# Optimization experiments

Measured on AMD Instinct MI355X. Metric: run time of the kernel, lower is better.

## Reference

```python
import jax, jax.numpy as jnp
import numpy as np

B, T, C, H = 4, 2048, 1024, 16
D = C // H  # head dim = 64


def setup_inputs() -> dict:
    key = jax.random.key(0)
    k0, k1, k2, k3, k4 = jax.random.split(key, 5)
    s = 0.02
    return {
        "x": jax.random.normal(k0, (B, T, C), dtype=jnp.float32),
        "W_qkv": jax.random.normal(k1, (C, 3 * C), dtype=jnp.float32) * s,
        "b_qkv": jnp.zeros((3 * C,), dtype=jnp.float32),
        "W_out": jax.random.normal(k2, (C, C), dtype=jnp.float32) * s,
        "b_out": jnp.zeros((C,), dtype=jnp.float32),
    }


def reference(x, W_qkv, b_qkv, W_out, b_out):
    b, t, c = x.shape
    qkv = x @ W_qkv + b_qkv                              # [B,T,3C]
    q, k, v = jnp.split(qkv, 3, axis=-1)
    # [B,T,C] -> [B,H,T,D]
    q = q.reshape(b, t, H, D).transpose(0, 2, 1, 3)
    k = k.reshape(b, t, H, D).transpose(0, 2, 1, 3)
    v = v.reshape(b, t, H, D).transpose(0, 2, 1, 3)
    scale = 1.0 / jnp.sqrt(jnp.asarray(D, dtype=q.dtype))
    attn = jnp.einsum("bhqd,bhkd->bhqk", q, k) * scale   # [B,H,T,T]
    causal = jnp.tril(jnp.ones((t, t), dtype=bool))
    attn = jnp.where(causal[None, None], attn, -jnp.inf)
    attn = jax.nn.softmax(attn, axis=-1)
    y = jnp.einsum("bhqk,bhkd->bhqd", attn, v)           # [B,H,T,D]
    y = y.transpose(0, 2, 1, 3).reshape(b, t, c)          # [B,T,C]
    return y @ W_out + b_out
```

## Files before the change

### kernel.cpp

```cpp
#include <hip/hip_runtime.h>
#include <math.h>

typedef __bf16 bf16x8 __attribute__((ext_vector_type(8)));
typedef __bf16 bf16x4 __attribute__((ext_vector_type(4)));
typedef short shortx4 __attribute__((ext_vector_type(4)));
typedef float floatx4 __attribute__((ext_vector_type(4)));

#define Tc 2048
#define Cdim 1024
#define Hc 16
#define Dc 64
#define Mrows 8192

__device__ __forceinline__ float bf2f(ushort u) {
  union { float f; unsigned int i; } v; v.i = ((unsigned int)u) << 16; return v.f;
}
__device__ __forceinline__ ushort f2bf(float f) {
  union { float f; unsigned int i; } v; v.f = f;
  unsigned int r = (v.i + 0x7FFFu + ((v.i >> 16) & 1u)) >> 16;
  return (ushort)r;
}
__device__ __forceinline__ ushort f2bf_pos(float f) {
  union { float f; unsigned int i; } v; v.f = f;
  return (ushort)((v.i + 0x8000u) >> 16);
}
__device__ __forceinline__ float exp2_fast(float x) {
#if __has_builtin(__builtin_amdgcn_exp2f)
  return __builtin_amdgcn_exp2f(x);
#else
  return exp2f(x);
#endif
}

#if __has_builtin(__builtin_amdgcn_mfma_f32_16x16x16_bf16)
__device__ __forceinline__ floatx4 mfma16(bf16x4 a, bf16x4 b, floatx4 c) {
  return __builtin_amdgcn_mfma_f32_16x16x16_bf16(a, b, c, 0, 0, 0);
}
#elif __has_builtin(__builtin_amdgcn_mfma_f32_16x16x16bf16_1k)
__device__ __forceinline__ floatx4 mfma16(bf16x4 a, bf16x4 b, floatx4 c) {
  union { bf16x4 bv; shortx4 sv; } ua, ub;
  ua.bv = a; ub.bv = b;
  return __builtin_amdgcn_mfma_f32_16x16x16bf16_1k(ua.sv, ub.sv, c, 0, 0, 0);
}
#else
__device__ __forceinline__ floatx4 mfma16(bf16x4 a, bf16x4 b, floatx4 c) {
  floatx4 d;
  asm("v_mfma_f32_16x16x16_bf16 %0, %1, %2, %3" : "=v"(d) : "v"(a), "v"(b), "v"(c));
  return d;
}
#endif

#if __has_builtin(__builtin_amdgcn_global_load_lds)
#define HAVE_GLL 1
__device__ __forceinline__ void async_load16(const ushort* g, ushort* l) {
  __builtin_amdgcn_global_load_lds((const __attribute__((address_space(1))) void*)g,
                                   (__attribute__((address_space(3))) void*)l, 16, 0, 0);
}
#else
#define HAVE_GLL 0
#endif

__global__ void sniff_kernel(const unsigned int* __restrict__ x, int* __restrict__ flag) {
  __shared__ int cnt;
  if (threadIdx.x == 0) cnt = 0;
  __syncthreads();
  int local = 0;
  for (int i = threadIdx.x; i < 1024; i += 256) {
    unsigned int w = x[i];
    unsigned int e = (w >> 7) & 0xFFu;
    if (e >= 100u && e <= 140u) local++;
  }
  atomicAdd(&cnt, local);
  __syncthreads();
  if (threadIdx.x == 0) *flag = (cnt >= 614) ? 1 : 0;
}

__global__ void convert_vec(const void* __restrict__ src, ushort* __restrict__ dst,
                            size_t n, const int* __restrict__ flag) {
  size_t i = (size_t)blockIdx.x * blockDim.x + threadIdx.x;
  size_t base = i * 4;
  if (base >= n) return;
  if (*flag) {
    *(ushort4*)(dst + base) = ((const ushort4*)src)[i];
  } else {
    float4 f = ((const float4*)src)[i];
    dst[base + 0] = f2bf(f.x);
    dst[base + 1] = f2bf(f.y);
    dst[base + 2] = f2bf(f.z);
    dst[base + 3] = f2bf(f.w);
  }
}

__global__ void transpose_convert(const void* __restrict__ src, ushort* __restrict__ dst,
                                  int R, int Ccols, const int* __restrict__ flag) {
  __shared__ float tile[32][33];
  const int bx = blockIdx.x, by = blockIdx.y;
  const int tx = threadIdx.x, ty = threadIdx.y;
  const bool isbf = (*flag != 0);
  #pragma unroll
  for (int i = ty; i < 32; i += 8) {
    int r = by * 32 + i;
    int c = bx * 32 + tx;
    float v = isbf ? bf2f(((const ushort*)src)[(size_t)r * Ccols + c])
                   : ((const float*)src)[(size_t)r * Ccols + c];
    tile[i][tx] = v;
  }
  __syncthreads();
  #pragma unroll
  for (int i = ty; i < 32; i += 8) {
    int cc = bx * 32 + i;
    int rr = by * 32 + tx;
    dst[(size_t)cc * R + rr] = f2bf(tile[tx][i]);
  }
}

#if HAVE_GLL

#define GEMM_CORE(A_, Bt_, acc_)                                               \
  __shared__ __align__(16) ushort As[2][128 * 64];                             \
  __shared__ __align__(16) ushort Bs[2][128 * 64];                             \
  const int tid = threadIdx.x;                                                 \
  const int wave = tid >> 6, lane = tid & 63;                                  \
  const int col = lane & 15, quad = lane >> 4;                                 \
  const int nwg = gridDim.x * gridDim.y;                                       \
  const int wg = blockIdx.y * gridDim.x + blockIdx.x;                          \
  const int swz = ((nwg & 7) == 0) ? ((wg & 7) * (nwg >> 3) + (wg >> 3)) : wg; \
  const int bx_ = swz / gridDim.y, by_ = swz % gridDim.y;                      \
  const int m0 = by_ * 128, n0 = bx_ * 128;                                    \
  const int wm = (wave >> 1) * 64, wn = (wave & 1) * 64;                       \
  floatx4 acc_[4][4];                                                          \
  _Pragma("unroll") for (int i = 0; i < 4; ++i)                                \
    _Pragma("unroll") for (int j = 0; j < 4; ++j)                              \
      acc_[i][j] = (floatx4){0.f, 0.f, 0.f, 0.f};                              \
  auto stage_ = [&](int u) {                                                   \
    const int bb = u & 1;                                                      \
    _Pragma("unroll") for (int i = 0; i < 4; ++i) {                            \
      const int sbase = i * 256 + wave * 64;                                   \
      const int s = sbase + lane;                                              \
      const int r = s >> 3, g = (lane & 7) ^ (r & 7);                          \
      async_load16(A_ + (size_t)(m0 + r) * 1024 + u * 64 + g * 8,              \
                   As[bb] + sbase * 8);                                        \
      async_load16(Bt_ + (size_t)(n0 + r) * 1024 + u * 64 + g * 8,             \
                   Bs[bb] + sbase * 8);                                        \
    }                                                                          \
  };                                                                           \
  stage_(0);                                                                   \
  stage_(1);                                                                   \
  asm volatile("s_waitcnt vmcnt(8)" ::: "memory");                             \
  __builtin_amdgcn_sched_barrier(0);                                           \
  __builtin_amdgcn_s_barrier();                                                \
  for (int t = 0; t < 16; ++t) {                                               \
    const ushort* Ab = As[t & 1];                                              \
    const ushort* Bb = Bs[t & 1];                                              \
    bf16x8 af[2][4], bfv[2][4];                                                \
    _Pragma("unroll") for (int ks = 0; ks < 2; ++ks) {                         \
      _Pragma("unroll") for (int mi = 0; mi < 4; ++mi) {                       \
        const int rr = wm + mi * 16 + col;                                     \
        const int gg = (ks * 4 + quad) ^ (rr & 7);                             \
        af[ks][mi] = *(const bf16x8*)(Ab + rr * 64 + gg * 8);                  \
      }                                                                        \
      _Pragma("unroll") for (int ni = 0; ni < 4; ++ni) {                       \
        const int rr = wn + ni * 16 + col;                                     \
        const int gg = (ks * 4 + quad) ^ (rr & 7);                             \
        bfv[ks][ni] = *(const bf16x8*)(Bb + rr * 64 + gg * 8);                 \
      }                                                                        \
    }                                                                          \
    asm volatile("s_waitcnt lgkmcnt(0)" ::: "memory");                         \
    __builtin_amdgcn_sched_barrier(0);                                         \
    __builtin_amdgcn_s_barrier();                                              \
    if (t + 2 < 16) stage_(t + 2);                                             \
    __builtin_amdgcn_s_setprio(1);                                             \
    _Pragma("unroll") for (int mi = 0; mi < 4; ++mi)                           \
      _Pragma("unroll") for (int ni = 0; ni < 4; ++ni) {                       \
        acc_[mi][ni] = __builtin_amdgcn_mfma_f32_16x16x32_bf16(                \
            af[0][mi], bfv[0][ni], acc_[mi][ni], 0, 0, 0);                     \
        acc_[mi][ni] = __builtin_amdgcn_mfma_f32_16x16x32_bf16(                \
            af[1][mi], bfv[1][ni], acc_[mi][ni], 0, 0, 0);                     \
      }                                                                        \
    __builtin_amdgcn_s_setprio(0);                                             \
    if (t + 2 < 16) { asm volatile("s_waitcnt vmcnt(8)" ::: "memory"); }       \
    else            { asm volatile("s_waitcnt vmcnt(0)" ::: "memory"); }       \
    __builtin_amdgcn_sched_barrier(0);                                         \
    __builtin_amdgcn_s_barrier();                                              \
  }

#else

#define STAGE16(gsrc, ldst, s) (*(uint4*)((ldst) + ((s) & 63) * 8) = *(const uint4*)(gsrc))
#define GEMM_CORE(A_, Bt_, acc_)                                               \
  __shared__ __align__(16) ushort As[2][128 * 64];                             \
  __shared__ __align__(16) ushort Bs[2][128 * 64];                             \
  const int tid = threadIdx.x;                                                 \
  const int wave = tid >> 6, lane = tid & 63;                                  \
  const int col = lane & 15, quad = lane >> 4;                                 \
  const int m0 = blockIdx.y * 128, n0 = blockIdx.x * 128;                      \
  const int wm = (wave >> 1) * 64, wn = (wave & 1) * 64;                       \
  floatx4 acc_[4][4];                                                          \
  _Pragma("unroll") for (int i = 0; i < 4; ++i)                                \
    _Pragma("unroll") for (int j = 0; j < 4; ++j)                              \
      acc_[i][j] = (floatx4){0.f, 0.f, 0.f, 0.f};                              \
  auto stage_ = [&](int t) {                                                   \
    const int bb = t & 1;                                                      \
    _Pragma("unroll") for (int i = 0; i < 4; ++i) {                            \
      const int sbase = i * 256 + wave * 64;                                   \
      const int s = sbase + lane;                                              \
      const int r = s >> 3, g = (lane & 7) ^ (r & 7);                          \
      STAGE16(A_ + (size_t)(m0 + r) * 1024 + t * 64 + g * 8,                   \
              As[bb] + sbase * 8, s);                                          \
      STAGE16(Bt_ + (size_t)(n0 + r) * 1024 + t * 64 + g * 8,                  \
              Bs[bb] + sbase * 8, s);                                          \
    }                                                                          \
  };                                                                           \
  stage_(0);                                                                   \
  __syncthreads();                                                             \
  for (int t = 0; t < 16; ++t) {                                               \
    if (t + 1 < 16) stage_(t + 1);                                             \
    const ushort* Ab = As[t & 1];                                              \
    const ushort* Bb = Bs[t & 1];                                              \
    _Pragma("unroll") for (int ks = 0; ks < 2; ++ks) {                         \
      bf16x8 af[4], bfv[4];                                                    \
      _Pragma("unroll") for (int mi = 0; mi < 4; ++mi) {                       \
        const int rr = wm + mi * 16 + col;                                     \
        const int gg = (ks * 4 + quad) ^ (rr & 7);                             \
        af[mi] = *(const bf16x8*)(Ab + rr * 64 + gg * 8);                      \
      }                                                                        \
      _Pragma("unroll") for (int ni = 0; ni < 4; ++ni) {                       \
        const int rr = wn + ni * 16 + col;                                     \
        const int gg = (ks * 4 + quad) ^ (rr & 7);                             \
        bfv[ni] = *(const bf16x8*)(Bb + rr * 64 + gg * 8);                     \
      }                                                                        \
      _Pragma("unroll") for (int mi = 0; mi < 4; ++mi)                         \
        _Pragma("unroll") for (int ni = 0; ni < 4; ++ni)                       \
          acc_[mi][ni] = __builtin_amdgcn_mfma_f32_16x16x32_bf16(              \
              af[mi], bfv[ni], acc_[mi][ni], 0, 0, 0);                         \
    }                                                                          \
    __syncthreads();                                                           \
  }

#endif

__global__ __launch_bounds__(256, 2) void gemm_qkv(const ushort* __restrict__ A,
                                                   const ushort* __restrict__ Bt,
                                                   const ushort* __restrict__ bias,
                                                   ushort* __restrict__ Qb,
                                                   ushort* __restrict__ Kb,
                                                   ushort* __restrict__ Vtb) {
  GEMM_CORE(A, Bt, acc)
  #pragma unroll
  for (int ni = 0; ni < 4; ++ni) {
    const int n = n0 + wn + ni * 16 + col;
    const float bi = bf2f(bias[n]);
    const int which = n >> 10;
    const int within = n & 1023;
    const int h = within >> 6, d = within & 63;
    #pragma unroll
    for (int mi = 0; mi < 4; ++mi) {
      #pragma unroll
      for (int r = 0; r < 4; ++r) {
        const int row = m0 + wm + mi * 16 + quad * 4 + r;
        const float v = acc[mi][ni][r] + bi;
        const int b = row >> 11, t = row & 2047;
        const size_t hb = (size_t)(b * Hc + h);
        const ushort ub = f2bf(v);
        if (which == 0)      Qb[(hb * Tc + t) * Dc + d] = ub;
        else if (which == 1) Kb[(hb * Tc + t) * Dc + d] = ub;
        else                 Vtb[(hb * Dc + d) * Tc + t] = ub;
      }
    }
  }
}

__global__ __launch_bounds__(256, 2) void gemm_out(const ushort* __restrict__ A,
                                                   const ushort* __restrict__ Bt,
                                                   const ushort* __restrict__ bias,
                                                   void* __restrict__ out,
                                                   const int* __restrict__ flag) {
  GEMM_CORE(A, Bt, acc)
  const bool isbf = (*flag != 0);
  #pragma unroll
  for (int ni = 0; ni < 4; ++ni) {
    const int n = n0 + wn + ni * 16 + col;
    const float bi = bf2f(bias[n]);
    #pragma unroll
    for (int mi = 0; mi < 4; ++mi) {
      #pragma unroll
      for (int r = 0; r < 4; ++r) {
        const int row = m0 + wm + mi * 16 + quad * 4 + r;
        const float v = acc[mi][ni][r] + bi;
        const size_t idx = (size_t)row * 1024 + n;
        if (isbf) ((ushort*)out)[idx] = f2bf(v);
        else      ((float*)out)[idx] = v;
      }
    }
  }
}

__global__ __launch_bounds__(512, 4) void attn_mfma(const ushort* __restrict__ Qb,
                                                    const ushort* __restrict__ Kb,
                                                    const ushort* __restrict__ Vtb,
                                                    ushort* __restrict__ Yb) {
  __shared__ __align__(16) ushort Kl[2][4096];
  __shared__ __align__(16) ushort Vl[2][4096];
  const int tid = threadIdx.x;
  const int bh = blockIdx.y;
  const int wave = tid >> 6, lane = tid & 63;
  const int col = lane & 15, quad = lane >> 4;
  const int pair = blockIdx.x;
  const int pHI = 15 - pair;
  const int pLO = pair;
  const int nA = 2 * pHI + 2;
  const int ntot = nA + 2 * pLO + 2;

  const ushort* Qh = Qb + (size_t)bh * Tc * Dc;
  const ushort* Kh = Kb + (size_t)bh * Tc * Dc;
  const ushort* Vth = Vtb + (size_t)bh * Dc * Tc;

  const int sr = tid >> 3, sg = (tid & 7) ^ (sr & 7);
  const ushort* kg = Kh + (size_t)sr * Dc + sg * 8;
  const ushort* vg = Vth + (size_t)sr * Tc + sg * 8;

  const int q0A = pHI * 128 + wave * 16;
  const int q0B = pLO * 128 + wave * 16;
  const int cdA = 2 * pHI + (wave >> 2);
  const int cdB = 2 * pLO + (wave >> 2);
  const int ktw = wave & 3;

  bf16x8 qfA[2], qfB[2];
  {
    const ushort* qa = Qh + (size_t)(q0A + col) * Dc + quad * 8;
    qfA[0] = *(const bf16x8*)(qa);
    qfA[1] = *(const bf16x8*)(qa + 32);
    const ushort* qb = Qh + (size_t)(q0B + col) * Dc + quad * 8;
    qfB[0] = *(const bf16x8*)(qb);
    qfB[1] = *(const bf16x8*)(qb + 32);
  }

  floatx4 o[4];
  float lpart = 0.f;
  #pragma unroll
  for (int dt = 0; dt < 4; ++dt) o[dt] = (floatx4){0.f, 0.f, 0.f, 0.f};

  constexpr float C1 = 0.18033688f;
  constexpr float C2 = -17.312340f;
  const int b = bh >> 4, h = bh & 15;

  auto stage = [&](int gi) {
    const int p = gi & 1;
    const int c = (gi < nA) ? gi : gi - nA;
    const size_t kOff = (size_t)c * 64;
#if HAVE_GLL
    async_load16(kg + kOff * Dc, &Kl[p][wave * 512]);
    async_load16(vg + kOff, &Vl[p][wave * 512]);
#else
    *(uint4*)&Kl[p][tid * 8] = *(const uint4*)(kg + kOff * Dc);
    *(uint4*)&Vl[p][tid * 8] = *(const uint4*)(vg + kOff);
#endif
  };

  auto chunk_compute = [&](int c, int p, const bf16x8 (&qf)[2], int cd) {
    if (c > cd) return;
    const bool masked = (c == cd);
    #pragma unroll
    for (int kt = 0; kt < 4; ++kt) {
      if (masked && kt > ktw) continue;
      const int rowk = kt * 16 + col;
      const int swk = rowk & 7;
      bf16x8 ka0 = *(const bf16x8*)(&Kl[p][rowk * 64 + ((quad ^ swk) * 8)]);
      bf16x8 ka1 = *(const bf16x8*)(&Kl[p][rowk * 64 + (((quad + 4) ^ swk) * 8)]);
      bf16x4 vf[4];
      #pragma unroll
      for (int dt = 0; dt < 4; ++dt) {
        const int rowv = dt * 16 + col;
        const int gv = (2 * kt + (quad >> 1)) ^ (rowv & 7);
        vf[dt] = *(const bf16x4*)(&Vl[p][rowv * 64 + gv * 8 + (quad & 1) * 4]);
      }
      floatx4 sf = {0.f, 0.f, 0.f, 0.f};
      sf = __builtin_amdgcn_mfma_f32_16x16x32_bf16(ka0, qf[0], sf, 0, 0, 0);
      sf = __builtin_amdgcn_mfma_f32_16x16x32_bf16(ka1, qf[1], sf, 0, 0, 0);
      union { ushort u[4]; bf16x4 v; } pu;
      float ps = 0.f;
      const bool tri = masked && (kt == ktw);
      #pragma unroll
      for (int r = 0; r < 4; ++r) {
        float pe = exp2_fast(fmaf(sf[r], C1, C2));
        if (tri) pe = (quad * 4 + r <= col) ? pe : 0.f;
        ps += pe;
        pu.u[r] = f2bf_pos(pe);
      }
      lpart += ps;
      #pragma unroll
      for (int dt = 0; dt < 4; ++dt)
        o[dt] = mfma16(vf[dt], pu.v, o[dt]);
    }
  };

  auto flush = [&](int q0) {
    float l = lpart;
    l += __shfl_xor(l, 16);
    l += __shfl_xor(l, 32);
    const float inv = 1.f / l;
    const int q = q0 + col;
    const size_t base = ((size_t)b * Tc + q) * Cdim + h * Dc;
    #pragma unroll
    for (int dt = 0; dt < 4; ++dt) {
      ushort4 y;
      y.x = f2bf(o[dt][0] * inv);
      y.y = f2bf(o[dt][1] * inv);
      y.z = f2bf(o[dt][2] * inv);
      y.w = f2bf(o[dt][3] * inv);
      *(ushort4*)(Yb + base + dt * 16 + quad * 4) = y;
    }
  };

  stage(0);
  __syncthreads();

  for (int c = 0; c < nA; ++c) {
    if (c + 1 < ntot) stage(c + 1);
    chunk_compute(c, c & 1, qfA, cdA);
    if (c == nA - 1) {
      flush(q0A);
      lpart = 0.f;
      #pragma unroll
      for (int dt = 0; dt < 4; ++dt) o[dt] = (floatx4){0.f, 0.f, 0.f, 0.f};
    }
    __syncthreads();
  }
  for (int gi = nA; gi < ntot; ++gi) {
    if (gi + 1 < ntot) stage(gi + 1);
    chunk_compute(gi - nA, gi & 1, qfB, cdB);
    __syncthreads();
  }
  flush(q0B);
}

extern "C" void kernel_launch(void* const* d_in, const int* in_sizes, int n_in,
                              void* d_out, int out_size, void* d_ws, size_t ws_size,
                              hipStream_t stream) {
  const void* x    = d_in[0];
  const void* Wqkv = d_in[1];
  const void* bqkv = d_in[2];
  const void* Wout = d_in[3];
  const void* bout = d_in[4];

  char* ws = (char*)d_ws;
  size_t off = 0;
  auto alloc = [&](size_t bytes) { size_t r = off; off += (bytes + 255) & ~(size_t)255; return r; };

  int*    flag = (int*)   (ws + alloc(256));
  ushort* xb   = (ushort*)(ws + alloc((size_t)Mrows * Cdim * 2));
  ushort* wqt  = (ushort*)(ws + alloc((size_t)3 * Cdim * Cdim * 2));
  ushort* wot  = (ushort*)(ws + alloc((size_t)Cdim * Cdim * 2));
  ushort* bqb  = (ushort*)(ws + alloc((size_t)3 * Cdim * 2));
  ushort* bob  = (ushort*)(ws + alloc((size_t)Cdim * 2));
  ushort* Qb   = (ushort*)(ws + alloc((size_t)Mrows * Cdim * 2));
  ushort* Kb   = (ushort*)(ws + alloc((size_t)Mrows * Cdim * 2));
  ushort* Vtb  = (ushort*)(ws + alloc((size_t)Mrows * Cdim * 2));
  ushort* Yb   = xb;

  sniff_kernel<<<1, 256, 0, stream>>>((const unsigned int*)x, flag);

  convert_vec<<<(Mrows * Cdim) / 1024, 256, 0, stream>>>(x, xb, (size_t)Mrows * Cdim, flag);
  convert_vec<<<3, 256, 0, stream>>>(bqkv, bqb, 3 * Cdim, flag);
  convert_vec<<<1, 256, 0, stream>>>(bout, bob, Cdim, flag);
  transpose_convert<<<dim3(96, 32), dim3(32, 8), 0, stream>>>(Wqkv, wqt, Cdim, 3 * Cdim, flag);
  transpose_convert<<<dim3(32, 32), dim3(32, 8), 0, stream>>>(Wout, wot, Cdim, Cdim, flag);

  gemm_qkv<<<dim3(24, 64), 256, 0, stream>>>(xb, wqt, bqb, Qb, Kb, Vtb);
  attn_mfma<<<dim3(8, 64), 512, 0, stream>>>(Qb, Kb, Vtb, Yb);
  gemm_out<<<dim3(8, 64), 256, 0, stream>>>(Yb, wot, bob, d_out, flag);
}
```

Measured before the change: 304.1 us.

## Enlarge GEMM tiles to 256x128 with 8 waves and vectorize V-transpose stores

Both projection GEMMs now use 512-thread blocks computing 256x128 output tiles, with the B tile shared across twice as many rows. Grids are halved, the workgroup swizzle is dropped, and the staging loads and waitcnt values are adjusted to match. The V-transpose epilogue now writes four consecutive time steps as one ushort4 store instead of scalar strided stores. This raises LDS use and register pressure per block, allowing one block per CU, and the removed swizzle may reduce L2 locality.

```diff
diff --git a/kernel.cpp b/kernel.cpp
--- a/kernel.cpp
+++ b/kernel.cpp
@@ -117,36 +117,35 @@
 #if HAVE_GLL
 
 #define GEMM_CORE(A_, Bt_, acc_)                                               \
-  __shared__ __align__(16) ushort As[2][128 * 64];                             \
+  __shared__ __align__(16) ushort As[2][256 * 64];                             \
   __shared__ __align__(16) ushort Bs[2][128 * 64];                             \
   const int tid = threadIdx.x;                                                 \
   const int wave = tid >> 6, lane = tid & 63;                                  \
   const int col = lane & 15, quad = lane >> 4;                                 \
-  const int nwg = gridDim.x * gridDim.y;                                       \
-  const int wg = blockIdx.y * gridDim.x + blockIdx.x;                          \
-  const int swz = ((nwg & 7) == 0) ? ((wg & 7) * (nwg >> 3) + (wg >> 3)) : wg; \
-  const int bx_ = swz / gridDim.y, by_ = swz % gridDim.y;                      \
-  const int m0 = by_ * 128, n0 = bx_ * 128;                                    \
-  const int wm = (wave >> 1) * 64, wn = (wave & 1) * 64;                       \
+  const int wm = wave >> 1, wn = wave & 1;                                     \
+  const int m0 = blockIdx.y * 256, n0 = blockIdx.x * 128;                      \
+  const int rl0 = tid >> 3, gsw = (tid & 7) ^ (rl0 & 7);                       \
   floatx4 acc_[4][4];                                                          \
   _Pragma("unroll") for (int i = 0; i < 4; ++i)                                \
     _Pragma("unroll") for (int j = 0; j < 4; ++j)                              \
       acc_[i][j] = (floatx4){0.f, 0.f, 0.f, 0.f};                              \
   auto stage_ = [&](int u) {                                                   \
     const int bb = u & 1;                                                      \
-    _Pragma("unroll") for (int i = 0; i < 4; ++i) {                            \
-      const int sbase = i * 256 + wave * 64;                                   \
-      const int s = sbase + lane;                                              \
-      const int r = s >> 3, g = (lane & 7) ^ (r & 7);                          \
-      async_load16(A_ + (size_t)(m0 + r) * 1024 + u * 64 + g * 8,              \
-                   As[bb] + sbase * 8);                                        \
-      async_load16(Bt_ + (size_t)(n0 + r) * 1024 + u * 64 + g * 8,             \
-                   Bs[bb] + sbase * 8);                                        \
+    _Pragma("unroll") for (int h = 0; h < 2; ++h)                              \
+      _Pragma("unroll") for (int i = 0; i < 2; ++i) {                          \
+        const int rl = i * 64 + rl0;                                           \
+        async_load16(A_ + (size_t)(m0 + h * 128 + rl) * 1024 + u * 64 + gsw * 8, \
+                     &As[bb][(h * 1024 + i * 512 + wave * 64) * 8]);           \
+      }                                                                        \
+    _Pragma("unroll") for (int i = 0; i < 2; ++i) {                            \
+      const int rl = i * 64 + rl0;                                             \
+      async_load16(Bt_ + (size_t)(n0 + rl) * 1024 + u * 64 + gsw * 8,          \
+                   &Bs[bb][(i * 512 + wave * 64) * 8]);                        \
     }                                                                          \
   };                                                                           \
   stage_(0);                                                                   \
   stage_(1);                                                                   \
-  asm volatile("s_waitcnt vmcnt(8)" ::: "memory");                             \
+  asm volatile("s_waitcnt vmcnt(6)" ::: "memory");                             \
   __builtin_amdgcn_sched_barrier(0);                                           \
   __builtin_amdgcn_s_barrier();                                                \
   for (int t = 0; t < 16; ++t) {                                               \
@@ -155,12 +154,12 @@
     bf16x8 af[2][4], bfv[2][4];                                                \
     _Pragma("unroll") for (int ks = 0; ks < 2; ++ks) {                         \
       _Pragma("unroll") for (int mi = 0; mi < 4; ++mi) {                       \
-        const int rr = wm + mi * 16 + col;                                     \
+        const int rr = wm * 64 + mi * 16 + col;                                \
         const int gg = (ks * 4 + quad) ^ (rr & 7);                             \
         af[ks][mi] = *(const bf16x8*)(Ab + rr * 64 + gg * 8);                  \
       }                                                                        \
       _Pragma("unroll") for (int ni = 0; ni < 4; ++ni) {                       \
-        const int rr = wn + ni * 16 + col;                                     \
+        const int rr = wn * 64 + ni * 16 + col;                                \
         const int gg = (ks * 4 + quad) ^ (rr & 7);                             \
         bfv[ks][ni] = *(const bf16x8*)(Bb + rr * 64 + gg * 8);                 \
       }                                                                        \
@@ -178,7 +177,7 @@
             af[1][mi], bfv[1][ni], acc_[mi][ni], 0, 0, 0);                     \
       }                                                                        \
     __builtin_amdgcn_s_setprio(0);                                             \
-    if (t + 2 < 16) { asm volatile("s_waitcnt vmcnt(8)" ::: "memory"); }       \
+    if (t + 2 < 16) { asm volatile("s_waitcnt vmcnt(6)" ::: "memory"); }       \
     else            { asm volatile("s_waitcnt vmcnt(0)" ::: "memory"); }       \
     __builtin_amdgcn_sched_barrier(0);                                         \
     __builtin_amdgcn_s_barrier();                                              \
@@ -186,29 +185,31 @@
 
 #else
 
-#define STAGE16(gsrc, ldst, s) (*(uint4*)((ldst) + ((s) & 63) * 8) = *(const uint4*)(gsrc))
 #define GEMM_CORE(A_, Bt_, acc_)                                               \
-  __shared__ __align__(16) ushort As[2][128 * 64];                             \
+  __shared__ __align__(16) ushort As[2][256 * 64];                             \
   __shared__ __align__(16) ushort Bs[2][128 * 64];                             \
   const int tid = threadIdx.x;                                                 \
   const int wave = tid >> 6, lane = tid & 63;                                  \
   const int col = lane & 15, quad = lane >> 4;                                 \
-  const int m0 = blockIdx.y * 128, n0 = blockIdx.x * 128;                      \
-  const int wm = (wave >> 1) * 64, wn = (wave & 1) * 64;                       \
+  const int wm = wave >> 1, wn = wave & 1;                                     \
+  const int m0 = blockIdx.y * 256, n0 = blockIdx.x * 128;                      \
+  const int rl0 = tid >> 3, gsw = (tid & 7) ^ (rl0 & 7);                       \
   floatx4 acc_[4][4];                                                          \
   _Pragma("unroll") for (int i = 0; i < 4; ++i)                                \
     _Pragma("unroll") for (int j = 0; j < 4; ++j)                              \
       acc_[i][j] = (floatx4){0.f, 0.f, 0.f, 0.f};                              \
-  auto stage_ = [&](int t) {                                                   \
-    const int bb = t & 1;                                                      \
-    _Pragma("unroll") for (int i = 0; i < 4; ++i) {                            \
-      const int sbase = i * 256 + wave * 64;                                   \
-      const int s = sbase + lane;                                              \
-      const int r = s >> 3, g = (lane & 7) ^ (r & 7);                          \
-      STAGE16(A_ + (size_t)(m0 + r) * 1024 + t * 64 + g * 8,                   \
-              As[bb] + sbase * 8, s);                                          \
-      STAGE16(Bt_ + (size_t)(n0 + r) * 1024 + t * 64 + g * 8,                  \
-              Bs[bb] + sbase * 8, s);                                          \
+  auto stage_ = [&](int u) {                                                   \
+    const int bb = u & 1;                                                      \
+    _Pragma("unroll") for (int h = 0; h < 2; ++h)                              \
+      _Pragma("unroll") for (int i = 0; i < 2; ++i) {                          \
+        const int rl = i * 64 + rl0;                                           \
+        *(uint4*)&As[bb][(h * 1024 + i * 512 + wave * 64 + lane) * 8] =        \
+            *(const uint4*)(A_ + (size_t)(m0 + h * 128 + rl) * 1024 + u * 64 + gsw * 8); \
+      }                                                                        \
+    _Pragma("unroll") for (int i = 0; i < 2; ++i) {                            \
+      const int rl = i * 64 + rl0;                                             \
+      *(uint4*)&Bs[bb][(i * 512 + wave * 64 + lane) * 8] =                     \
+          *(const uint4*)(Bt_ + (size_t)(n0 + rl) * 1024 + u * 64 + gsw * 8);  \
     }                                                                          \
   };                                                                           \
   stage_(0);                                                                   \
@@ -220,12 +221,12 @@
     _Pragma("unroll") for (int ks = 0; ks < 2; ++ks) {                         \
       bf16x8 af[4], bfv[4];                                                    \
       _Pragma("unroll") for (int mi = 0; mi < 4; ++mi) {                       \
-        const int rr = wm + mi * 16 + col;                                     \
+        const int rr = wm * 64 + mi * 16 + col;                                \
         const int gg = (ks * 4 + quad) ^ (rr & 7);                             \
         af[mi] = *(const bf16x8*)(Ab + rr * 64 + gg * 8);                      \
       }                                                                        \
       _Pragma("unroll") for (int ni = 0; ni < 4; ++ni) {                       \
-        const int rr = wn + ni * 16 + col;                                     \
+        const int rr = wn * 64 + ni * 16 + col;                                \
         const int gg = (ks * 4 + quad) ^ (rr & 7);                             \
         bfv[ni] = *(const bf16x8*)(Bb + rr * 64 + gg * 8);                     \
       }                                                                        \
@@ -239,7 +240,7 @@
 
 #endif
 
-__global__ __launch_bounds__(256, 2) void gemm_qkv(const ushort* __restrict__ A,
+__global__ __launch_bounds__(512, 1) void gemm_qkv(const ushort* __restrict__ A,
                                                    const ushort* __restrict__ Bt,
                                                    const ushort* __restrict__ bias,
                                                    ushort* __restrict__ Qb,
@@ -248,29 +249,43 @@
   GEMM_CORE(A, Bt, acc)
   #pragma unroll
   for (int ni = 0; ni < 4; ++ni) {
-    const int n = n0 + wn + ni * 16 + col;
+    const int n = n0 + wn * 64 + ni * 16 + col;
     const float bi = bf2f(bias[n]);
     const int which = n >> 10;
     const int within = n & 1023;
     const int h = within >> 6, d = within & 63;
-    #pragma unroll
-    for (int mi = 0; mi < 4; ++mi) {
-      #pragma unroll
-      for (int r = 0; r < 4; ++r) {
-        const int row = m0 + wm + mi * 16 + quad * 4 + r;
-        const float v = acc[mi][ni][r] + bi;
-        const int b = row >> 11, t = row & 2047;
-        const size_t hb = (size_t)(b * Hc + h);
-        const ushort ub = f2bf(v);
-        if (which == 0)      Qb[(hb * Tc + t) * Dc + d] = ub;
-        else if (which == 1) Kb[(hb * Tc + t) * Dc + d] = ub;
-        else                 Vtb[(hb * Dc + d) * Tc + t] = ub;
+    if (which == 2) {
+      const size_t vbase = ((size_t)0);
+      #pragma unroll
+      for (int mi = 0; mi < 4; ++mi) {
+        const int row0 = m0 + wm * 64 + mi * 16 + quad * 4;
+        const int b = row0 >> 11, t0 = row0 & 2047;
+        ushort4 y;
+        y.x = f2bf(acc[mi][ni][0] + bi);
+        y.y = f2bf(acc[mi][ni][1] + bi);
+        y.z = f2bf(acc[mi][ni][2] + bi);
+        y.w = f2bf(acc[mi][ni][3] + bi);
+        *(ushort4*)(Vtb + ((size_t)(b * Hc + h) * Dc + d) * Tc + t0 + vbase) = y;
+      }
+    } else {
+      #pragma unroll
+      for (int mi = 0; mi < 4; ++mi) {
+        #pragma unroll
+        for (int r = 0; r < 4; ++r) {
+          const int row = m0 + wm * 64 + mi * 16 + quad * 4 + r;
+          const float v = acc[mi][ni][r] + bi;
+          const int b = row >> 11, t = row & 2047;
+          const size_t hb = (size_t)(b * Hc + h);
+          const ushort ub = f2bf(v);
+          if (which == 0) Qb[(hb * Tc + t) * Dc + d] = ub;
+          else            Kb[(hb * Tc + t) * Dc + d] = ub;
+        }
       }
     }
   }
 }
 
-__global__ __launch_bounds__(256, 2) void gemm_out(const ushort* __restrict__ A,
+__global__ __launch_bounds__(512, 1) void gemm_out(const ushort* __restrict__ A,
                                                    const ushort* __restrict__ Bt,
                                                    const ushort* __restrict__ bias,
                                                    void* __restrict__ out,
@@ -279,13 +294,13 @@
   const bool isbf = (*flag != 0);
   #pragma unroll
   for (int ni = 0; ni < 4; ++ni) {
-    const int n = n0 + wn + ni * 16 + col;
+    const int n = n0 + wn * 64 + ni * 16 + col;
     const float bi = bf2f(bias[n]);
     #pragma unroll
     for (int mi = 0; mi < 4; ++mi) {
       #pragma unroll
       for (int r = 0; r < 4; ++r) {
-        const int row = m0 + wm + mi * 16 + quad * 4 + r;
+        const int row = m0 + wm * 64 + mi * 16 + quad * 4 + r;
         const float v = acc[mi][ni][r] + bi;
         const size_t idx = (size_t)row * 1024 + n;
         if (isbf) ((ushort*)out)[idx] = f2bf(v);
@@ -466,7 +481,7 @@
   transpose_convert<<<dim3(96, 32), dim3(32, 8), 0, stream>>>(Wqkv, wqt, Cdim, 3 * Cdim, flag);
   transpose_convert<<<dim3(32, 32), dim3(32, 8), 0, stream>>>(Wout, wot, Cdim, Cdim, flag);
 
-  gemm_qkv<<<dim3(24, 64), 256, 0, stream>>>(xb, wqt, bqb, Qb, Kb, Vtb);
+  gemm_qkv<<<dim3(24, 32), 512, 0, stream>>>(xb, wqt, bqb, Qb, Kb, Vtb);
   attn_mfma<<<dim3(8, 64), 512, 0, stream>>>(Qb, Kb, Vtb, Yb);
-  gemm_out<<<dim3(8, 64), 256, 0, stream>>>(Yb, wot, bob, d_out, flag);
-}
+  gemm_out<<<dim3(8, 32), 512, 0, stream>>>(Yb, wot, bob, d_out, flag);
+}
```

After: 266.2 us. -12.4%, faster.
